# Optimization experiments

Hardware: AMD Instinct MI355X
Metric: run time of the kernel (lower is better)

The kernel has to match this reference:

```python
import jax, jax.numpy as jnp
import numpy as np

DEPTH, DIM, DFF, VOCAB = 4, 512, 2048, 4096
EPS = 1e-5

def layernorm(x, w, b):
    mu = jnp.mean(x, axis=-1, keepdims=True)
    var = jnp.mean((x - mu) ** 2, axis=-1, keepdims=True)
    return (x - mu) * jax.lax.rsqrt(var + EPS) * w + b

def sconv(x, phazor_c, last_conv_c):
    # x: [B,L,dim] real; phazor_c, last_conv_c: [dim] complex
    B, L, D = x.shape
    r = jnp.abs(phazor_c)
    p = jnp.tanh(r) * jnp.exp(1j * jnp.angle(phazor_c))          # [dim]
    prog = p[None, :] ** jnp.arange(L, dtype=jnp.float32)[:, None]  # [L,dim]
    filt_fft = jnp.fft.fft(prog, n=2 * L, axis=0)                # [2L,dim]
    x_fft = jnp.fft.fft(x.astype(jnp.complex64), n=2 * L, axis=1)  # [B,2L,dim]
    conv = jnp.fft.ifft(filt_fft[None] * x_fft, axis=1)[:, :L]   # [B,L,dim]
    conv = conv + last_conv_c[None, None, :] * prog[None] * p[None, None, :]
    return conv.real.astype(x.dtype)

def setup_inputs() -> dict:
    key = jax.random.key(0)
    ks = jax.random.split(key, 20)
    f32 = jnp.float32
    inp = {}
    inp['x'] = jax.random.normal(ks[0], (2, 4096, VOCAB), dtype=f32)
    inp['Win'] = jax.random.normal(ks[1], (DIM, VOCAB), dtype=f32) * VOCAB ** -0.5
    inp['bin'] = jnp.zeros((DIM,), f32)
    inp['ln1_w'] = jnp.ones((DEPTH, DIM), f32)
    inp['ln1_b'] = jnp.zeros((DEPTH, DIM), f32)
    # phazor init: exp(2*pi*i*arange/dim)*|randn|
    ang = 2 * np.pi * jnp.arange(DIM, dtype=f32) / DIM
    mag = jnp.abs(jax.random.normal(ks[2], (DEPTH, DIM), dtype=f32))
    inp['phz_re'] = mag * jnp.cos(ang)[None]
    inp['phz_im'] = mag * jnp.sin(ang)[None]
    inp['lc_re'] = jax.random.normal(ks[3], (DEPTH, DIM), dtype=f32)
    inp['lc_im'] = jax.random.normal(ks[4], (DEPTH, DIM), dtype=f32)
    inp['sc_lin'] = jnp.ones((DEPTH, DIM), f32)
    inp['ln2_w'] = jnp.ones((DEPTH, DIM), f32)
    inp['ln2_b'] = jnp.zeros((DEPTH, DIM), f32)
    inp['W1'] = jax.random.normal(ks[5], (DEPTH, DFF, DIM), dtype=f32) * DIM ** -0.5
    inp['b1'] = jnp.zeros((DEPTH, DFF), f32)
    inp['W2'] = jax.random.normal(ks[6], (DEPTH, DIM, DFF), dtype=f32) * DFF ** -0.5
    inp['b2'] = jnp.zeros((DEPTH, DIM), f32)
    inp['lnl_w'] = jnp.ones((DIM,), f32)
    inp['lnl_b'] = jnp.zeros((DIM,), f32)
    inp['Wout'] = jax.random.normal(ks[7], (VOCAB, DIM), dtype=f32) * DIM ** -0.5
    inp['bout'] = jnp.zeros((VOCAB,), f32)
    return inp

def _forward(x, Win, bin, ln1_w, ln1_b, phz_re, phz_im, lc_re, lc_im, sc_lin,
             ln2_w, ln2_b, W1, b1, W2, b2, lnl_w, lnl_b, Wout, bout):
    h = jnp.einsum('blv,dv->bld', x, Win) + bin  # token_in

    def body(h, p):
        l1w, l1b, pr, pi, lr, li, scl, l2w, l2b, w1, b1_, w2, b2_ = p
        y = jax.nn.silu(layernorm(h, l1w, l1b))
        y = sconv(y, pr + 1j * pi, lr + 1j * li)
        h = h + y * scl
        y = layernorm(h, l2w, l2b)
        y = jax.nn.silu(jnp.einsum('bld,fd->blf', y, w1) + b1_)
        y = jnp.einsum('blf,df->bld', y, w2) + b2_
        return h + y, None

    xs = (ln1_w, ln1_b, phz_re, phz_im, lc_re, lc_im, sc_lin,
          ln2_w, ln2_b, W1, b1, W2, b2)
    h, _ = jax.lax.scan(body, h, xs)
    h = layernorm(h, lnl_w, lnl_b)
    return jnp.einsum('bld,vd->blv', h, Wout) + bout

def reference(x, Win, bin, ln1_w, ln1_b, phz_re, phz_im, lc_re, lc_im, sc_lin,
              ln2_w, ln2_b, W1, b1, W2, b2, lnl_w, lnl_b, Wout, bout):
    return _forward(x, Win, bin, ln1_w, ln1_b, phz_re, phz_im, lc_re, lc_im,
                    sc_lin, ln2_w, ln2_b, W1, b1, W2, b2, lnl_w, lnl_b, Wout, bout)
```

## Files before the change

kernel.cpp:

```cpp
#include <hip/hip_runtime.h>
#include <hip/hip_bf16.h>
#include <cstdint>
#include <cstddef>

#define DEPTH 4
#define DIM 512
#define DFF 2048
#define VOCAB 4096
#define NB 2
#define LSEQ 4096
#define MR (NB*LSEQ)
#define EPSL 1e-5f
#define NC 128
#define TCH 32

typedef __attribute__((ext_vector_type(8))) short  s8v;
typedef __attribute__((ext_vector_type(4))) float  f4v;
typedef __attribute__((ext_vector_type(8))) __bf16 bf8v;

__device__ __forceinline__ unsigned short f2b(float f) {
  union { float f; unsigned int u; } v; v.f = f;
  unsigned int r = v.u + 0x7FFFu + ((v.u >> 16) & 1u);
  return (unsigned short)(r >> 16);
}

__device__ __forceinline__ void gld16(const void* g, void* l) {
  __builtin_amdgcn_global_load_lds(
      (const __attribute__((address_space(1))) unsigned int*)(uintptr_t)g,
      (__attribute__((address_space(3))) unsigned int*)(uintptr_t)l,
      16, 0, 0);
}

__global__ void __launch_bounds__(256) cvt_f32_bf16(
    const float* __restrict__ in, unsigned short* __restrict__ out, int n8)
{
  int i = blockIdx.x * 256 + threadIdx.x;
  if (i >= n8) return;
  const f4v* p = (const f4v*)(in + (size_t)i * 8);
  f4v a = p[0], b = p[1];
  s8v o;
  o[0]=(short)f2b(a[0]); o[1]=(short)f2b(a[1]); o[2]=(short)f2b(a[2]); o[3]=(short)f2b(a[3]);
  o[4]=(short)f2b(b[0]); o[5]=(short)f2b(b[1]); o[6]=(short)f2b(b[2]); o[7]=(short)f2b(b[3]);
  *(s8v*)(out + (size_t)i * 8) = o;
}

template<int MODE>
__global__ void __launch_bounds__(256) ln_kernel(
    const float* __restrict__ x, const float* __restrict__ w, const float* __restrict__ b,
    float* __restrict__ outf, unsigned short* __restrict__ outb)
{
  int row  = blockIdx.x * 4 + (threadIdx.x >> 6);
  int lane = threadIdx.x & 63;
  const float* xp = x + (size_t)row * DIM + lane * 8;
  f4v v0 = *(const f4v*)xp;
  f4v v1 = *(const f4v*)(xp + 4);
  float s = 0.f, s2 = 0.f;
#pragma unroll
  for (int j = 0; j < 4; ++j) { s += v0[j]; s2 += v0[j]*v0[j]; s += v1[j]; s2 += v1[j]*v1[j]; }
#pragma unroll
  for (int off = 32; off; off >>= 1) { s += __shfl_xor(s, off, 64); s2 += __shfl_xor(s2, off, 64); }
  float mu = s * (1.f / DIM);
  float rs = rsqrtf(s2 * (1.f / DIM) - mu * mu + EPSL);
  int c = lane * 8;
  f4v w0 = *(const f4v*)(w + c), w1 = *(const f4v*)(w + c + 4);
  f4v b0 = *(const f4v*)(b + c), b1 = *(const f4v*)(b + c + 4);
  float ov[8];
#pragma unroll
  for (int j = 0; j < 8; ++j) {
    float xv = (j < 4) ? v0[j] : v1[j - 4];
    float wv = (j < 4) ? w0[j] : w1[j - 4];
    float bv = (j < 4) ? b0[j] : b1[j - 4];
    float o = (xv - mu) * rs * wv + bv;
    if (MODE == 0) o = o / (1.f + __expf(-o));
    ov[j] = o;
  }
  if (MODE == 0) {
    f4v o0 = {ov[0], ov[1], ov[2], ov[3]};
    f4v o1 = {ov[4], ov[5], ov[6], ov[7]};
    *(f4v*)(outf + (size_t)row * DIM + c)     = o0;
    *(f4v*)(outf + (size_t)row * DIM + c + 4) = o1;
  } else {
    s8v o;
#pragma unroll
    for (int j = 0; j < 8; ++j) o[j] = (short)f2b(ov[j]);
    *(s8v*)(outb + (size_t)row * DIM + c) = o;
  }
}

__device__ __forceinline__ void phz2p(float re, float im, float& pre, float& pim) {
  float r = sqrtf(re * re + im * im);
  float t = (r > 1e-20f) ? (tanhf(r) / r) : 1.0f;
  pre = t * re; pim = t * im;
}

__global__ void __launch_bounds__(256) scan_a(
    const float* __restrict__ y, const float* __restrict__ pr, const float* __restrict__ pi,
    float* __restrict__ stA)
{
  int d = blockIdx.z * 256 + threadIdx.x;
  int b = blockIdx.y, c = blockIdx.x;
  float pre, pim; phz2p(pr[d], pi[d], pre, pim);
  const float* yp = y + ((size_t)b * LSEQ + (size_t)c * TCH) * DIM + d;
  float sre = 0.f, sim = 0.f;
#pragma unroll 8
  for (int j = 0; j < TCH; ++j) {
    float xv = yp[(size_t)j * DIM];
    float nre = fmaf(pre, sre, fmaf(-pim, sim, xv));
    float nim = fmaf(pre, sim, pim * sre);
    sre = nre; sim = nim;
  }
  size_t o = (((size_t)b * NC + c) * DIM + d) * 2;
  stA[o] = sre; stA[o + 1] = sim;
}

__global__ void __launch_bounds__(256) scan_b(
    const float* __restrict__ stA, float* __restrict__ carry,
    const float* __restrict__ pr, const float* __restrict__ pi,
    const float* __restrict__ lcr, const float* __restrict__ lci)
{
  int idx = blockIdx.x * 256 + threadIdx.x;
  int b = idx >> 9, d = idx & (DIM - 1);
  float pre, pim; phz2p(pr[d], pi[d], pre, pim);
  float qre = pre, qim = pim;
#pragma unroll
  for (int t = 0; t < 5; ++t) { float nr = qre*qre - qim*qim; float ni = 2.f*qre*qim; qre = nr; qim = ni; }
  float cre = lcr[d], cim = lci[d];
#pragma unroll 4
  for (int c = 0; c < NC; ++c) {
    size_t o = (((size_t)b * NC + c) * DIM + d) * 2;
    carry[o] = cre; carry[o + 1] = cim;
    float are = stA[o], aim = stA[o + 1];
    float nr = fmaf(qre, cre, fmaf(-qim, cim, are));
    float ni = fmaf(qre, cim, fmaf(qim, cre, aim));
    cre = nr; cim = ni;
  }
}

__global__ void __launch_bounds__(256) scan_c(
    const float* __restrict__ y, float* __restrict__ h, const float* __restrict__ carry,
    const float* __restrict__ pr, const float* __restrict__ pi,
    const float* __restrict__ scl)
{
  int d = blockIdx.z * 256 + threadIdx.x;
  int b = blockIdx.y, c = blockIdx.x;
  float pre, pim; phz2p(pr[d], pi[d], pre, pim);
  size_t o = (((size_t)b * NC + c) * DIM + d) * 2;
  float sre = carry[o], sim = carry[o + 1];
  float sc = scl[d];
  const float* yp = y + ((size_t)b * LSEQ + (size_t)c * TCH) * DIM + d;
  float*       hp = h + ((size_t)b * LSEQ + (size_t)c * TCH) * DIM + d;
#pragma unroll 8
  for (int j = 0; j < TCH; ++j) {
    float xv = yp[(size_t)j * DIM];
    float nre = fmaf(pre, sre, fmaf(-pim, sim, xv));
    float nim = fmaf(pre, sim, pim * sre);
    sre = nre; sim = nim;
    hp[(size_t)j * DIM] += sre * sc;
  }
}

template<int EPI, int AF32>
__global__ void __launch_bounds__(256, 4) gemm_bt(
    const void* __restrict__ Ap, const unsigned short* __restrict__ Bm,
    const float* __restrict__ bias,
    float* __restrict__ Cf, unsigned short* __restrict__ Cb,
    int N, int Keff, int lda, int ldb)
{
  __shared__ unsigned short As[2][128 * 32];
  __shared__ unsigned short Bs[2][128 * 32];
  const int tid  = threadIdx.x;
  const int lane = tid & 63, wave = tid >> 6;
  const int wm = wave >> 1, wn = wave & 1;
  const int fr = lane & 15, fq = lane >> 4;
  const int bz = blockIdx.z;

  int bx, by;
  {
    int gx = gridDim.x;
    int nwg = gx * gridDim.y;
    int b = blockIdx.y * gx + blockIdx.x;
    int lid = (b & 7) * (nwg >> 3) + (b >> 3);
    bx = lid % gx; by = lid / gx;
  }
  const int m0 = by * 128, n0 = bx * 128;
  const int koff = bz * Keff;

  f4v acc[4][4];
#pragma unroll
  for (int i = 0; i < 4; ++i)
#pragma unroll
    for (int j = 0; j < 4; ++j) acc[i][j] = (f4v){0.f, 0.f, 0.f, 0.f};

  const int nkt = Keff >> 5;

  f4v areg[2][2];
  auto loadA = [&](int k0) {
    const float* Ab = (const float*)Ap + (size_t)m0 * lda + koff + k0;
#pragma unroll
    for (int r = 0; r < 2; ++r) {
      int idx = r * 256 + tid;
      int row = idx >> 2, col = (idx & 3) << 3;
      const float* p = Ab + (size_t)row * lda + col;
      areg[r][0] = *(const f4v*)p;
      areg[r][1] = *(const f4v*)(p + 4);
    }
  };
  auto writeA = [&](int buf) {
#pragma unroll
    for (int r = 0; r < 2; ++r) {
      int idx = r * 256 + tid;
      s8v o;
#pragma unroll
      for (int j = 0; j < 4; ++j) {
        o[j]     = (short)f2b(areg[r][0][j]);
        o[4 + j] = (short)f2b(areg[r][1][j]);
      }
      *(s8v*)&As[buf][idx * 8] = o;
    }
  };
  auto stageA16 = [&](int buf, int k0) {
    const unsigned short* Ab = (const unsigned short*)Ap + (size_t)m0 * lda + koff + k0;
#pragma unroll
    for (int r = 0; r < 2; ++r) {
      int idx = r * 256 + tid;
      int row = idx >> 2, col = (idx & 3) << 3;
      gld16(Ab + (size_t)row * lda + col, &As[buf][idx * 8]);
    }
  };
  auto stageB = [&](int buf, int k0) {
    const unsigned short* Bb = Bm + (size_t)n0 * ldb + koff + k0;
#pragma unroll
    for (int r = 0; r < 2; ++r) {
      int idx = r * 256 + tid;
      int row = idx >> 2, col = (idx & 3) << 3;
      gld16(Bb + (size_t)row * ldb + col, &Bs[buf][idx * 8]);
    }
  };

  if constexpr (AF32) loadA(0); else stageA16(0, 0);
  stageB(0, 0);
  if constexpr (AF32) writeA(0);
  __syncthreads();

  for (int kt = 0; kt < nkt; ++kt) {
    int cur = kt & 1;
    bool pf = (kt + 1 < nkt);
    if (pf) {
      if constexpr (AF32) loadA((kt + 1) << 5);
      else stageA16(cur ^ 1, (kt + 1) << 5);
      stageB(cur ^ 1, (kt + 1) << 5);
    }
    bf8v av[4], bv[4];
#pragma unroll
    for (int i = 0; i < 4; ++i)
      av[i] = *(const bf8v*)&As[cur][(wm * 64 + i * 16 + fr) * 32 + fq * 8];
#pragma unroll
    for (int j = 0; j < 4; ++j)
      bv[j] = *(const bf8v*)&Bs[cur][(wn * 64 + j * 16 + fr) * 32 + fq * 8];
#pragma unroll
    for (int i = 0; i < 4; ++i)
#pragma unroll
      for (int j = 0; j < 4; ++j)
        acc[i][j] = __builtin_amdgcn_mfma_f32_16x16x32_bf16(av[i], bv[j], acc[i][j], 0, 0, 0);
    if (pf) { if constexpr (AF32) writeA(cur ^ 1); }
    __syncthreads();
  }

  const size_t pbase = (EPI == 3) ? (size_t)bz * MR * N : 0;
#pragma unroll
  for (int j = 0; j < 4; ++j) {
    const int col = n0 + wn * 64 + j * 16 + fr;
    const float bsv = (EPI == 3) ? 0.f : bias[col];
#pragma unroll
    for (int i = 0; i < 4; ++i) {
#pragma unroll
      for (int r = 0; r < 4; ++r) {
        const int row = m0 + wm * 64 + i * 16 + fq * 4 + r;
        const size_t off = (size_t)row * N + col;
        float v = acc[i][j][r] + bsv;
        if constexpr (EPI == 0) {
          Cf[off] = v;
        } else if constexpr (EPI == 1) {
          float sv = v / (1.f + __expf(-v));
          Cb[off] = f2b(sv);
        } else {
          Cf[pbase + off] = v;
        }
      }
    }
  }
}

template<int RES>
__global__ void __launch_bounds__(256) reduce_sk(
    const float* __restrict__ parts, const float* __restrict__ bias,
    float* __restrict__ out)
{
  size_t i = ((size_t)blockIdx.x * 256 + threadIdx.x) * 4;
  const size_t st = (size_t)MR * DIM;
  f4v v = *(const f4v*)(parts + i);
  v += *(const f4v*)(parts + st + i);
  v += *(const f4v*)(parts + 2 * st + i);
  v += *(const f4v*)(parts + 3 * st + i);
  int c = (int)(i & (DIM - 1));
  v += *(const f4v*)(bias + c);
  if (RES) v += *(const f4v*)(out + i);
  *(f4v*)(out + i) = v;
}

extern "C" void kernel_launch(void* const* d_in, const int* in_sizes, int n_in,
                              void* d_out, int out_size, void* d_ws, size_t ws_size,
                              hipStream_t stream)
{
  (void)in_sizes; (void)n_in; (void)out_size; (void)ws_size;
  const float* x    = (const float*)d_in[0];
  const float* Win  = (const float*)d_in[1];
  const float* bin  = (const float*)d_in[2];
  const float* ln1w = (const float*)d_in[3];
  const float* ln1b = (const float*)d_in[4];
  const float* phzr = (const float*)d_in[5];
  const float* phzi = (const float*)d_in[6];
  const float* lcr  = (const float*)d_in[7];
  const float* lci  = (const float*)d_in[8];
  const float* scl  = (const float*)d_in[9];
  const float* ln2w = (const float*)d_in[10];
  const float* ln2b = (const float*)d_in[11];
  const float* W1   = (const float*)d_in[12];
  const float* b1   = (const float*)d_in[13];
  const float* W2   = (const float*)d_in[14];
  const float* b2   = (const float*)d_in[15];
  const float* lnlw = (const float*)d_in[16];
  const float* lnlb = (const float*)d_in[17];
  const float* Wout = (const float*)d_in[18];
  const float* bout = (const float*)d_in[19];

  char* wsp = (char*)d_ws;
  auto alloc = [&](size_t bytes) { char* p = wsp; wsp += (bytes + 255) & ~(size_t)255; return p; };
  float*          h     = (float*)alloc((size_t)MR * DIM * 4);
  float*          y     = (float*)alloc((size_t)MR * DIM * 4);
  unsigned short* yb    = (unsigned short*)alloc((size_t)MR * DIM * 2);
  unsigned short* Winb  = (unsigned short*)alloc((size_t)DIM * VOCAB * 2);
  unsigned short* W1b   = (unsigned short*)alloc((size_t)DEPTH * DFF * DIM * 2);
  unsigned short* W2b   = (unsigned short*)alloc((size_t)DEPTH * DIM * DFF * 2);
  unsigned short* Woutb = (unsigned short*)alloc((size_t)VOCAB * DIM * 2);
  float*          stA   = (float*)alloc((size_t)NB * NC * DIM * 2 * 4);
  float*          carry = (float*)alloc((size_t)NB * NC * DIM * 2 * 4);

  unsigned short* act1  = (unsigned short*)d_out;
  float*          parts = (float*)((char*)d_out + ((size_t)40 << 20));

  dim3 blk(256);
  cvt_f32_bf16<<<dim3((DIM * VOCAB) / 2048), blk, 0, stream>>>(Win, Winb, DIM * VOCAB / 8);
  cvt_f32_bf16<<<dim3((DEPTH * DFF * DIM) / 2048), blk, 0, stream>>>(W1, W1b, DEPTH * DFF * DIM / 8);
  cvt_f32_bf16<<<dim3((DEPTH * DFF * DIM) / 2048), blk, 0, stream>>>(W2, W2b, DEPTH * DIM * DFF / 8);
  cvt_f32_bf16<<<dim3((VOCAB * DIM) / 2048), blk, 0, stream>>>(Wout, Woutb, VOCAB * DIM / 8);

  gemm_bt<3, 1><<<dim3(DIM / 128, MR / 128, 4), blk, 0, stream>>>(
      x, Winb, nullptr, parts, nullptr, DIM, VOCAB / 4, VOCAB, VOCAB);
  reduce_sk<0><<<dim3(MR * DIM / 1024), blk, 0, stream>>>(parts, bin, h);

  for (int l = 0; l < DEPTH; ++l) {
    ln_kernel<0><<<dim3(MR / 4), blk, 0, stream>>>(h, ln1w + l * DIM, ln1b + l * DIM, y, nullptr);
    scan_a<<<dim3(NC, NB, DIM / 256), blk, 0, stream>>>(y, phzr + l * DIM, phzi + l * DIM, stA);
    scan_b<<<dim3((NB * DIM) / 256), blk, 0, stream>>>(stA, carry, phzr + l * DIM, phzi + l * DIM,
                                                       lcr + l * DIM, lci + l * DIM);
    scan_c<<<dim3(NC, NB, DIM / 256), blk, 0, stream>>>(y, h, carry, phzr + l * DIM, phzi + l * DIM,
                                                        scl + l * DIM);
    ln_kernel<1><<<dim3(MR / 4), blk, 0, stream>>>(h, ln2w + l * DIM, ln2b + l * DIM, nullptr, yb);
    gemm_bt<1, 0><<<dim3(DFF / 128, MR / 128, 1), blk, 0, stream>>>(
        yb, W1b + (size_t)l * DFF * DIM, b1 + l * DFF, nullptr, act1, DFF, DIM, DIM, DIM);
    gemm_bt<3, 0><<<dim3(DIM / 128, MR / 128, 4), blk, 0, stream>>>(
        act1, W2b + (size_t)l * DIM * DFF, nullptr, parts, nullptr, DIM, DFF / 4, DFF, DFF);
    reduce_sk<1><<<dim3(MR * DIM / 1024), blk, 0, stream>>>(parts, b2 + l * DIM, h);
  }
  ln_kernel<1><<<dim3(MR / 4), blk, 0, stream>>>(h, lnlw, lnlb, nullptr, yb);
  gemm_bt<0, 0><<<dim3(VOCAB / 128, MR / 128, 1), blk, 0, stream>>>(
      yb, Woutb, bout, (float*)d_out, nullptr, VOCAB, DIM, DIM, DIM);
}
```

Before: 668.5 us.

## Triple-buffer GEMM with vmcnt waits and pre-convert input to bf16

```diff
diff --git a/kernel.cpp b/kernel.cpp
--- a/kernel.cpp
+++ b/kernel.cpp
@@ -29,6 +29,12 @@
       (const __attribute__((address_space(1))) unsigned int*)(uintptr_t)g,
       (__attribute__((address_space(3))) unsigned int*)(uintptr_t)l,
       16, 0, 0);
+}
+
+template<int N> __device__ __forceinline__ void wvm() {
+  if constexpr (N == 8)      asm volatile("s_waitcnt vmcnt(8)" ::: "memory");
+  else if constexpr (N == 4) asm volatile("s_waitcnt vmcnt(4)" ::: "memory");
+  else                       asm volatile("s_waitcnt vmcnt(0)" ::: "memory");
 }
 
 __global__ void __launch_bounds__(256) cvt_f32_bf16(
@@ -159,15 +165,15 @@
   }
 }
 
-template<int EPI, int AF32>
-__global__ void __launch_bounds__(256, 4) gemm_bt(
-    const void* __restrict__ Ap, const unsigned short* __restrict__ Bm,
+template<int EPI>
+__global__ void __launch_bounds__(256, 3) gemm_p(
+    const unsigned short* __restrict__ A, const unsigned short* __restrict__ Bm,
     const float* __restrict__ bias,
     float* __restrict__ Cf, unsigned short* __restrict__ Cb,
     int N, int Keff, int lda, int ldb)
 {
-  __shared__ unsigned short As[2][128 * 32];
-  __shared__ unsigned short Bs[2][128 * 32];
+  __shared__ unsigned short As[3][128 * 32];
+  __shared__ unsigned short Bs[3][128 * 32];
   const int tid  = threadIdx.x;
   const int lane = tid & 63, wave = tid >> 6;
   const int wm = wave >> 1, wn = wave & 1;
@@ -184,6 +190,7 @@
   }
   const int m0 = by * 128, n0 = bx * 128;
   const int koff = bz * Keff;
+  const int nkt = Keff >> 5;
 
   f4v acc[4][4];
 #pragma unroll
@@ -191,79 +198,43 @@
 #pragma unroll
     for (int j = 0; j < 4; ++j) acc[i][j] = (f4v){0.f, 0.f, 0.f, 0.f};
 
-  const int nkt = Keff >> 5;
-
-  f4v areg[2][2];
-  auto loadA = [&](int k0) {
-    const float* Ab = (const float*)Ap + (size_t)m0 * lda + koff + k0;
-#pragma unroll
-    for (int r = 0; r < 2; ++r) {
-      int idx = r * 256 + tid;
-      int row = idx >> 2, col = (idx & 3) << 3;
-      const float* p = Ab + (size_t)row * lda + col;
-      areg[r][0] = *(const f4v*)p;
-      areg[r][1] = *(const f4v*)(p + 4);
-    }
+  const int row2 = tid >> 2, col2 = (tid & 3) << 3;
+  auto stage = [&](int buf, int kt) {
+    const unsigned short* Ab = A  + (size_t)m0 * lda + koff + kt * 32;
+    const unsigned short* Bb = Bm + (size_t)n0 * ldb + koff + kt * 32;
+    gld16(Ab + (size_t)row2 * lda + col2,        &As[buf][tid * 8]);
+    gld16(Ab + (size_t)(row2 + 64) * lda + col2, &As[buf][(256 + tid) * 8]);
+    gld16(Bb + (size_t)row2 * ldb + col2,        &Bs[buf][tid * 8]);
+    gld16(Bb + (size_t)(row2 + 64) * ldb + col2, &Bs[buf][(256 + tid) * 8]);
   };
-  auto writeA = [&](int buf) {
-#pragma unroll
-    for (int r = 0; r < 2; ++r) {
-      int idx = r * 256 + tid;
-      s8v o;
-#pragma unroll
-      for (int j = 0; j < 4; ++j) {
-        o[j]     = (short)f2b(areg[r][0][j]);
-        o[4 + j] = (short)f2b(areg[r][1][j]);
-      }
-      *(s8v*)&As[buf][idx * 8] = o;
-    }
-  };
-  auto stageA16 = [&](int buf, int k0) {
-    const unsigned short* Ab = (const unsigned short*)Ap + (size_t)m0 * lda + koff + k0;
-#pragma unroll
-    for (int r = 0; r < 2; ++r) {
-      int idx = r * 256 + tid;
-      int row = idx >> 2, col = (idx & 3) << 3;
-      gld16(Ab + (size_t)row * lda + col, &As[buf][idx * 8]);
-    }
-  };
-  auto stageB = [&](int buf, int k0) {
-    const unsigned short* Bb = Bm + (size_t)n0 * ldb + koff + k0;
-#pragma unroll
-    for (int r = 0; r < 2; ++r) {
-      int idx = r * 256 + tid;
-      int row = idx >> 2, col = (idx & 3) << 3;
-      gld16(Bb + (size_t)row * ldb + col, &Bs[buf][idx * 8]);
-    }
-  };
-
-  if constexpr (AF32) loadA(0); else stageA16(0, 0);
-  stageB(0, 0);
-  if constexpr (AF32) writeA(0);
-  __syncthreads();
-
+
+  stage(0, 0);
+  stage(1, 1);
+
+  int b0 = 0, b1 = 1, b2 = 2;
   for (int kt = 0; kt < nkt; ++kt) {
-    int cur = kt & 1;
-    bool pf = (kt + 1 < nkt);
-    if (pf) {
-      if constexpr (AF32) loadA((kt + 1) << 5);
-      else stageA16(cur ^ 1, (kt + 1) << 5);
-      stageB(cur ^ 1, (kt + 1) << 5);
-    }
+    bool pf = (kt + 2 < nkt);
+    if (pf) stage(b2, kt + 2);
+    if (pf)                    wvm<8>();
+    else if (kt + 1 < nkt)     wvm<4>();
+    else                       wvm<0>();
+    __builtin_amdgcn_s_barrier();
+    __builtin_amdgcn_sched_barrier(0);
     bf8v av[4], bv[4];
 #pragma unroll
     for (int i = 0; i < 4; ++i)
-      av[i] = *(const bf8v*)&As[cur][(wm * 64 + i * 16 + fr) * 32 + fq * 8];
+      av[i] = *(const bf8v*)&As[b0][(wm * 64 + i * 16 + fr) * 32 + fq * 8];
 #pragma unroll
     for (int j = 0; j < 4; ++j)
-      bv[j] = *(const bf8v*)&Bs[cur][(wn * 64 + j * 16 + fr) * 32 + fq * 8];
+      bv[j] = *(const bf8v*)&Bs[b0][(wn * 64 + j * 16 + fr) * 32 + fq * 8];
 #pragma unroll
     for (int i = 0; i < 4; ++i)
 #pragma unroll
       for (int j = 0; j < 4; ++j)
         acc[i][j] = __builtin_amdgcn_mfma_f32_16x16x32_bf16(av[i], bv[j], acc[i][j], 0, 0, 0);
-    if (pf) { if constexpr (AF32) writeA(cur ^ 1); }
-    __syncthreads();
+    __builtin_amdgcn_sched_barrier(0);
+    __builtin_amdgcn_s_barrier();
+    int t = b0; b0 = b1; b1 = b2; b2 = t;
   }
 
   const size_t pbase = (EPI == 3) ? (size_t)bz * MR * N : 0;
@@ -346,17 +317,19 @@
   float*          stA   = (float*)alloc((size_t)NB * NC * DIM * 2 * 4);
   float*          carry = (float*)alloc((size_t)NB * NC * DIM * 2 * 4);
 
+  unsigned short* xb    = (unsigned short*)d_out;
   unsigned short* act1  = (unsigned short*)d_out;
-  float*          parts = (float*)((char*)d_out + ((size_t)40 << 20));
+  float*          parts = (float*)((char*)d_out + ((size_t)64 << 20));
 
   dim3 blk(256);
+  cvt_f32_bf16<<<dim3(((size_t)MR * VOCAB) / 2048), blk, 0, stream>>>(x, xb, (int)(((size_t)MR * VOCAB) / 8));
   cvt_f32_bf16<<<dim3((DIM * VOCAB) / 2048), blk, 0, stream>>>(Win, Winb, DIM * VOCAB / 8);
   cvt_f32_bf16<<<dim3((DEPTH * DFF * DIM) / 2048), blk, 0, stream>>>(W1, W1b, DEPTH * DFF * DIM / 8);
   cvt_f32_bf16<<<dim3((DEPTH * DFF * DIM) / 2048), blk, 0, stream>>>(W2, W2b, DEPTH * DIM * DFF / 8);
   cvt_f32_bf16<<<dim3((VOCAB * DIM) / 2048), blk, 0, stream>>>(Wout, Woutb, VOCAB * DIM / 8);
 
-  gemm_bt<3, 1><<<dim3(DIM / 128, MR / 128, 4), blk, 0, stream>>>(
-      x, Winb, nullptr, parts, nullptr, DIM, VOCAB / 4, VOCAB, VOCAB);
+  gemm_p<3><<<dim3(DIM / 128, MR / 128, 4), blk, 0, stream>>>(
+      xb, Winb, nullptr, parts, nullptr, DIM, VOCAB / 4, VOCAB, VOCAB);
   reduce_sk<0><<<dim3(MR * DIM / 1024), blk, 0, stream>>>(parts, bin, h);
 
   for (int l = 0; l < DEPTH; ++l) {
@@ -367,13 +340,13 @@
     scan_c<<<dim3(NC, NB, DIM / 256), blk, 0, stream>>>(y, h, carry, phzr + l * DIM, phzi + l * DIM,
                                                         scl + l * DIM);
     ln_kernel<1><<<dim3(MR / 4), blk, 0, stream>>>(h, ln2w + l * DIM, ln2b + l * DIM, nullptr, yb);
-    gemm_bt<1, 0><<<dim3(DFF / 128, MR / 128, 1), blk, 0, stream>>>(
+    gemm_p<1><<<dim3(DFF / 128, MR / 128, 1), blk, 0, stream>>>(
         yb, W1b + (size_t)l * DFF * DIM, b1 + l * DFF, nullptr, act1, DFF, DIM, DIM, DIM);
-    gemm_bt<3, 0><<<dim3(DIM / 128, MR / 128, 4), blk, 0, stream>>>(
+    gemm_p<3><<<dim3(DIM / 128, MR / 128, 4), blk, 0, stream>>>(
         act1, W2b + (size_t)l * DIM * DFF, nullptr, parts, nullptr, DIM, DFF / 4, DFF, DFF);
     reduce_sk<1><<<dim3(MR * DIM / 1024), blk, 0, stream>>>(parts, b2 + l * DIM, h);
   }
   ln_kernel<1><<<dim3(MR / 4), blk, 0, stream>>>(h, lnlw, lnlb, nullptr, yb);
-  gemm_bt<0, 0><<<dim3(VOCAB / 128, MR / 128, 1), blk, 0, stream>>>(
+  gemm_p<0><<<dim3(VOCAB / 128, MR / 128, 1), blk, 0, stream>>>(
       yb, Woutb, bout, (float*)d_out, nullptr, VOCAB, DIM, DIM, DIM);
 }
```

Result: faster. 646.8 us (-3.3%).
